# Performance work log

Hardware: AMD Instinct MI355X
Metric: run time of the kernel (lower is better)

Reference implementation:

```python
import jax, jax.numpy as jnp
import numpy as np

B, DIN, DOUT, NC = 8192, 4096, 4096, 64


def setup_inputs() -> dict:
    key = jax.random.key(0)
    k1, k2, k3, k4, k5 = jax.random.split(key, 5)
    x = jax.random.normal(k1, (B, DIN), dtype=jnp.float32)
    cluster = jax.random.uniform(k2, (B, NC), dtype=jnp.float32)
    weight = jax.random.uniform(k3, (DIN, DOUT), dtype=jnp.float32,
                                minval=-0.25, maxval=0.25)
    # torch init is ones; perturb slightly so the modulation is non-trivial
    style_L = 1.0 + 0.1 * jax.random.normal(k4, (NC, DIN), dtype=jnp.float32)
    style_R = 1.0 + 0.1 * jax.random.normal(k5, (NC, DOUT), dtype=jnp.float32)
    return {"x": x, "cluster": cluster, "weight": weight,
            "style_L": style_L, "style_R": style_R}


def reference(x, cluster, weight, style_L, style_R):
    # tmp_L: (B, din), tmp_R: (B, dout)
    tmp_L = cluster @ style_L
    tmp_R = cluster @ style_R
    # Algebraically identical to (weight * outer(tmp_L, tmp_R)) applied per
    # sample: out[b,o] = sum_i x[b,i]*tmpL[b,i]*W[i,o]*tmpR[b,o].
    # Factorized form avoids the (B, din, dout) intermediate.
    return ((x * tmp_L) @ weight) * tmp_R
```

## Files before the change

kernel.cpp:

```cpp
#include <hip/hip_runtime.h>
#include <cstdint>

#define BB   8192
#define DIN  4096
#define DOUT 4096
#define NCL  64

typedef __bf16 bf16;
typedef __attribute__((ext_vector_type(8)))  __bf16 bf16x8;
typedef __attribute__((ext_vector_type(4)))  float  f32x4;
typedef __attribute__((ext_vector_type(16))) float  f32x16;

#define GAS(p) (reinterpret_cast<uint32_t __attribute__((address_space(1)))*>(reinterpret_cast<uintptr_t>(p)))
#define LAS(p) (reinterpret_cast<uint32_t __attribute__((address_space(3)))*>(reinterpret_cast<uintptr_t>(p)))

#define WAITV(n)  asm volatile("s_waitcnt vmcnt(" #n ")" ::: "memory")
#define WAITLN(n) asm volatile("s_waitcnt lgkmcnt(" #n ")" ::: "memory")
#define WAITL()   asm volatile("s_waitcnt lgkmcnt(0)" ::: "memory")
#define BARR()    __builtin_amdgcn_s_barrier()
#define SCHED0()  __builtin_amdgcn_sched_barrier(0)
#define MFMA16(a, b, c) __builtin_amdgcn_mfma_f32_16x16x32_bf16((a), (b), (c), 0, 0, 0)
#define MFMA32(a, b, c) __builtin_amdgcn_mfma_f32_32x32x16_bf16((a), (b), (c), 0, 0, 0)

__global__ __launch_bounds__(256) void prologue_kernel(
    const float* __restrict__ x, const float* __restrict__ cl,
    const float* __restrict__ sL, bf16* __restrict__ Ap,
    bf16* __restrict__ clb)
{
    __shared__ uint4 lds_u4[2048];
    char* lds = (char*)lds_u4;
    const int t    = threadIdx.x;
    const int lane = t & 63;
    const int w    = t >> 6;
    const int wm   = w >> 1, wn = w & 1;
    const int r0   = blockIdx.x * 128;
    const int c0   = blockIdx.y * 128;

    #pragma unroll
    for (int i = 0; i < 4; i++) {
        int tk  = t + i * 256;
        int row = tk >> 3, ch = tk & 7;
        const float* src = cl + (size_t)(r0 + row) * NCL + ch * 8;
        float4 v0 = *(const float4*)src;
        float4 v1 = *(const float4*)(src + 4);
        bf16x8 pk;
        pk[0]=(bf16)v0.x; pk[1]=(bf16)v0.y; pk[2]=(bf16)v0.z; pk[3]=(bf16)v0.w;
        pk[4]=(bf16)v1.x; pk[5]=(bf16)v1.y; pk[6]=(bf16)v1.z; pk[7]=(bf16)v1.w;
        *(bf16x8*)(lds + row * 128 + ((ch ^ (row & 7)) << 4)) = pk;
        if (blockIdx.y == 0)
            *(bf16x8*)(clb + (size_t)(r0 + row) * NCL + ch * 8) = pk;
    }
    #pragma unroll
    for (int i = 0; i < 4; i++) {
        int tk = t + i * 256;
        int n  = tk & 127, c = tk >> 7;
        bf16x8 pl;
        #pragma unroll
        for (int j = 0; j < 8; j++)
            pl[j] = (bf16)sL[(size_t)(c * 8 + j) * DIN + c0 + n];
        *(bf16x8*)(lds + 16384 + n * 128 + ((c ^ (n & 7)) << 4)) = pl;
    }
    __syncthreads();

    f32x4 accL[4][4] = {};
    #pragma unroll
    for (int s = 0; s < 2; s++) {
        bf16x8 a[4], bl[4];
        #pragma unroll
        for (int m = 0; m < 4; m++) {
            int row = wm * 64 + m * 16 + (lane & 15);
            int ch  = s * 4 + (lane >> 4);
            a[m] = *(bf16x8*)(lds + row * 128 + ((ch ^ (row & 7)) << 4));
        }
        #pragma unroll
        for (int n = 0; n < 4; n++) {
            int row = wn * 64 + n * 16 + (lane & 15);
            int ch  = s * 4 + (lane >> 4);
            bl[n] = *(bf16x8*)(lds + 16384 + row * 128 + ((ch ^ (row & 7)) << 4));
        }
        #pragma unroll
        for (int m = 0; m < 4; m++)
            #pragma unroll
            for (int n = 0; n < 4; n++)
                accL[m][n] = MFMA16(a[m], bl[n], accL[m][n]);
    }

    #pragma unroll
    for (int m = 0; m < 4; m++) {
        int rbase = r0 + wm * 64 + m * 16 + ((lane >> 4) << 2);
        #pragma unroll
        for (int n = 0; n < 4; n++) {
            int col = c0 + wn * 64 + n * 16 + (lane & 15);
            #pragma unroll
            for (int j = 0; j < 4; j++) {
                size_t idx = (size_t)(rbase + j) * DIN + col;
                Ap[idx] = (bf16)(x[idx] * accL[m][n][j]);
            }
        }
    }
}

__global__ __launch_bounds__(256) void transpose_kernel(
    const float* __restrict__ W, bf16* __restrict__ Wt)
{
    const int t  = threadIdx.x;
    const int n  = blockIdx.x * 256 + t;
    const int k0 = blockIdx.y * 32;
    bf16x8 v[4];
    #pragma unroll
    for (int q = 0; q < 4; q++)
        #pragma unroll
        for (int j = 0; j < 8; j++)
            v[q][j] = (bf16)W[(size_t)(k0 + q * 8 + j) * DOUT + n];
    bf16* dst = Wt + (size_t)n * DIN + k0;
    #pragma unroll
    for (int q = 0; q < 4; q++)
        *(bf16x8*)(dst + q * 8) = v[q];
}

__global__ __launch_bounds__(256) void srt_kernel(
    const float* __restrict__ sR, bf16* __restrict__ srt)
{
    const int o = blockIdx.x * 256 + threadIdx.x;
    bf16x8 v[8];
    #pragma unroll
    for (int q = 0; q < 8; q++)
        #pragma unroll
        for (int j = 0; j < 8; j++)
            v[q][j] = (bf16)sR[(size_t)(q * 8 + j) * DOUT + o];
    bf16* dst = srt + (size_t)o * 64;
    #pragma unroll
    for (int q = 0; q < 8; q++)
        *(bf16x8*)(dst + q * 8) = v[q];
}

template<int CUR>
__device__ __forceinline__ void tile_step(char* lds, int tid,
    const bf16* pA1, const bf16* pA2, const bf16* pA3, const bf16* pA4,
    const bf16* pB1, const bf16* pB2, const bf16* pB3, const bf16* pB4,
    int kA1, int kA2, int arow, int brow,
    int ks0, int ks1, int ks2, int ks3,
    bf16x8 (&a)[2][4], bf16x8 (&b0)[4], bf16x8 (&b1)[4], f32x16 (&acc)[4][2])
{
    constexpr int CB = CUR * 65536;
    constexpr int OB = (CUR ^ 1) * 65536;
    const int ks[4] = {ks0, ks1, ks2, ks3};

    #pragma unroll
    for (int f = 0; f < 2; ++f)
        #pragma unroll
        for (int kk = 0; kk < 4; ++kk)
            a[f][kk] = *(const bf16x8*)(lds + CB + f * 4096 + arow + ks[kk]);
    #pragma unroll
    for (int kk = 0; kk < 4; ++kk)
        b0[kk] = *(const bf16x8*)(lds + CB + 32768 + brow + ks[kk]);
    __builtin_amdgcn_global_load_lds(GAS(pA3 + kA1), LAS(lds + OB + 16384 + tid * 16), 16, 0, 0);
    __builtin_amdgcn_global_load_lds(GAS(pA4 + kA1), LAS(lds + OB + 24576 + tid * 16), 16, 0, 0);
    WAITLN(8);
    BARR();
    WAITL(); SCHED0();
    __builtin_amdgcn_s_setprio(1);
    #pragma unroll
    for (int kk = 0; kk < 4; ++kk)
        #pragma unroll
        for (int f = 0; f < 2; ++f)
            acc[f][0] = MFMA32(a[f][kk], b0[kk], acc[f][0]);
    __builtin_amdgcn_s_setprio(0);
    BARR();

    #pragma unroll
    for (int kk = 0; kk < 4; ++kk)
        b1[kk] = *(const bf16x8*)(lds + CB + 49152 + brow + ks[kk]);
    __builtin_amdgcn_global_load_lds(GAS(pA1 + kA2), LAS(lds + CB + tid * 16), 16, 0, 0);
    __builtin_amdgcn_global_load_lds(GAS(pA2 + kA2), LAS(lds + CB + 8192 + tid * 16), 16, 0, 0);
    BARR();
    WAITL(); SCHED0();
    __builtin_amdgcn_s_setprio(1);
    #pragma unroll
    for (int kk = 0; kk < 4; ++kk)
        #pragma unroll
        for (int f = 0; f < 2; ++f)
            acc[f][1] = MFMA32(a[f][kk], b1[kk], acc[f][1]);
    __builtin_amdgcn_s_setprio(0);
    BARR();

    #pragma unroll
    for (int f = 0; f < 2; ++f)
        #pragma unroll
        for (int kk = 0; kk < 4; ++kk)
            a[f][kk] = *(const bf16x8*)(lds + CB + 16384 + f * 4096 + arow + ks[kk]);
    __builtin_amdgcn_global_load_lds(GAS(pB1 + kA2), LAS(lds + CB + 32768 + tid * 16), 16, 0, 0);
    __builtin_amdgcn_global_load_lds(GAS(pB2 + kA2), LAS(lds + CB + 40960 + tid * 16), 16, 0, 0);
    BARR();
    WAITL(); SCHED0();
    __builtin_amdgcn_s_setprio(1);
    #pragma unroll
    for (int kk = 0; kk < 4; ++kk)
        #pragma unroll
        for (int f = 0; f < 2; ++f)
            acc[2 + f][1] = MFMA32(a[f][kk], b1[kk], acc[2 + f][1]);
    __builtin_amdgcn_s_setprio(0);
    BARR();

    __builtin_amdgcn_global_load_lds(GAS(pB3 + kA2), LAS(lds + CB + 49152 + tid * 16), 16, 0, 0);
    __builtin_amdgcn_global_load_lds(GAS(pB4 + kA2), LAS(lds + CB + 57344 + tid * 16), 16, 0, 0);
    BARR();
    __builtin_amdgcn_s_setprio(1);
    #pragma unroll
    for (int kk = 0; kk < 4; ++kk)
        #pragma unroll
        for (int f = 0; f < 2; ++f)
            acc[2 + f][0] = MFMA32(a[f][kk], b0[kk], acc[2 + f][0]);
    __builtin_amdgcn_s_setprio(0);
    WAITV(6);
    BARR();
}

__global__ __launch_bounds__(512, 2) void gemm_kernel(
    const bf16* __restrict__ Ap, const bf16* __restrict__ Wt,
    const bf16* __restrict__ clb, const bf16* __restrict__ srt,
    float* __restrict__ out)
{
    __shared__ uint4 smem[8192];
    char* lds = (char*)smem;
    const int tid  = threadIdx.x;
    const int lane = tid & 63;
    const int w    = tid >> 6;
    const int wm   = w >> 2;
    const int wn   = w & 3;
    const int L5 = lane & 31, H1 = lane >> 5;

    const int bid = blockIdx.x;
    const int xc  = bid & 7, ii = bid >> 3;
    const int mt  = xc * 4 + (ii >> 4);
    const int nt  = ii & 15;
    const size_t brow_g = (size_t)mt * 256;
    const size_t bcol_g = (size_t)nt * 256;

    const int r1  = tid >> 3;
    const int gch = (tid & 7) ^ (r1 & 7);
    const bf16* pA1 = Ap + (brow_g + r1) * (size_t)DIN + gch * 8;
    const bf16* pA2 = pA1 + (size_t)64  * DIN;
    const bf16* pA3 = pA1 + (size_t)128 * DIN;
    const bf16* pA4 = pA1 + (size_t)192 * DIN;
    const bf16* pB1 = Wt + (bcol_g + r1) * (size_t)DIN + gch * 8;
    const bf16* pB2 = pB1 + (size_t)64  * DIN;
    const bf16* pB3 = pB1 + (size_t)128 * DIN;
    const bf16* pB4 = pB1 + (size_t)192 * DIN;

    const int ks0 = (((0 * 2 + H1) ^ (L5 & 7)) << 4);
    const int ks1 = (((1 * 2 + H1) ^ (L5 & 7)) << 4);
    const int ks2 = (((2 * 2 + H1) ^ (L5 & 7)) << 4);
    const int ks3 = (((3 * 2 + H1) ^ (L5 & 7)) << 4);
    const int arow = (wm * 64 + L5) * 128;
    const int brow = (wn * 32 + L5) * 128;

    bf16x8 a[2][4], b0[4], b1[4];
    f32x16 acc[4][2] = {};

    __builtin_amdgcn_global_load_lds(GAS(pA1), LAS(lds + tid * 16), 16, 0, 0);
    __builtin_amdgcn_global_load_lds(GAS(pA2), LAS(lds + 8192 + tid * 16), 16, 0, 0);
    __builtin_amdgcn_global_load_lds(GAS(pA3), LAS(lds + 16384 + tid * 16), 16, 0, 0);
    __builtin_amdgcn_global_load_lds(GAS(pA4), LAS(lds + 24576 + tid * 16), 16, 0, 0);
    __builtin_amdgcn_global_load_lds(GAS(pB1), LAS(lds + 32768 + tid * 16), 16, 0, 0);
    __builtin_amdgcn_global_load_lds(GAS(pB2), LAS(lds + 40960 + tid * 16), 16, 0, 0);
    __builtin_amdgcn_global_load_lds(GAS(pB3), LAS(lds + 49152 + tid * 16), 16, 0, 0);
    __builtin_amdgcn_global_load_lds(GAS(pB4), LAS(lds + 57344 + tid * 16), 16, 0, 0);
    __builtin_amdgcn_global_load_lds(GAS(pA1 + 64), LAS(lds + 65536 + tid * 16), 16, 0, 0);
    __builtin_amdgcn_global_load_lds(GAS(pA2 + 64), LAS(lds + 65536 + 8192 + tid * 16), 16, 0, 0);
    __builtin_amdgcn_global_load_lds(GAS(pB1 + 64), LAS(lds + 65536 + 32768 + tid * 16), 16, 0, 0);
    __builtin_amdgcn_global_load_lds(GAS(pB2 + 64), LAS(lds + 65536 + 40960 + tid * 16), 16, 0, 0);
    __builtin_amdgcn_global_load_lds(GAS(pB3 + 64), LAS(lds + 65536 + 49152 + tid * 16), 16, 0, 0);
    __builtin_amdgcn_global_load_lds(GAS(pB4 + 64), LAS(lds + 65536 + 57344 + tid * 16), 16, 0, 0);
    WAITV(6);
    BARR();

    #pragma unroll 1
    for (int t = 0; t < 64; t += 2) {
        tile_step<0>(lds, tid, pA1, pA2, pA3, pA4, pB1, pB2, pB3, pB4,
                     ((t + 1) & 63) * 64, ((t + 2) & 63) * 64,
                     arow, brow, ks0, ks1, ks2, ks3, a, b0, b1, acc);
        tile_step<1>(lds, tid, pA1, pA2, pA3, pA4, pB1, pB2, pB3, pB4,
                     ((t + 2) & 63) * 64, ((t + 3) & 63) * 64,
                     arow, brow, ks0, ks1, ks2, ks3, a, b0, b1, acc);
    }

    WAITV(0);
    const bf16* pC = clb + (brow_g + r1) * 64 + gch * 8;
    const bf16* pR = srt + (bcol_g + r1) * 64 + gch * 8;
    __builtin_amdgcn_global_load_lds(GAS(pC),         LAS(lds + tid * 16), 16, 0, 0);
    __builtin_amdgcn_global_load_lds(GAS(pC + 4096),  LAS(lds + 8192 + tid * 16), 16, 0, 0);
    __builtin_amdgcn_global_load_lds(GAS(pC + 8192),  LAS(lds + 16384 + tid * 16), 16, 0, 0);
    __builtin_amdgcn_global_load_lds(GAS(pC + 12288), LAS(lds + 24576 + tid * 16), 16, 0, 0);
    __builtin_amdgcn_global_load_lds(GAS(pR),         LAS(lds + 32768 + tid * 16), 16, 0, 0);
    __builtin_amdgcn_global_load_lds(GAS(pR + 4096),  LAS(lds + 40960 + tid * 16), 16, 0, 0);
    __builtin_amdgcn_global_load_lds(GAS(pR + 8192),  LAS(lds + 49152 + tid * 16), 16, 0, 0);
    __builtin_amdgcn_global_load_lds(GAS(pR + 12288), LAS(lds + 57344 + tid * 16), 16, 0, 0);
    WAITV(0);
    BARR();

    const int ks[4] = {ks0, ks1, ks2, ks3};
    bf16x8 cb[2][4];
    #pragma unroll
    for (int nf = 0; nf < 2; ++nf)
        #pragma unroll
        for (int kk = 0; kk < 4; ++kk)
            cb[nf][kk] = *(const bf16x8*)(lds + 32768 + (nf * 2 + (wn >> 1)) * 8192
                                          + ((wn & 1) * 32 + L5) * 128 + ks[kk]);
    #pragma unroll
    for (int mf = 0; mf < 4; ++mf) {
        bf16x8 ca[4];
        #pragma unroll
        for (int kk = 0; kk < 4; ++kk)
            ca[kk] = *(const bf16x8*)(lds + ((mf >> 1) * 2 + wm) * 8192
                                      + ((mf & 1) * 32 + L5) * 128 + ks[kk]);
        WAITL(); SCHED0();
        #pragma unroll
        for (int nf = 0; nf < 2; ++nf) {
            f32x16 r = {};
            #pragma unroll
            for (int kk = 0; kk < 4; ++kk)
                r = MFMA32(ca[kk], cb[nf][kk], r);
            acc[mf][nf] *= r;
        }
    }

    #pragma unroll
    for (int mf = 0; mf < 4; ++mf) {
        size_t rbase = brow_g + (size_t)((mf >> 1) * 128 + wm * 64 + (mf & 1) * 32 + 4 * H1);
        #pragma unroll
        for (int nf = 0; nf < 2; ++nf) {
            size_t col = bcol_g + (size_t)(nf * 128 + wn * 32 + L5);
            #pragma unroll
            for (int reg = 0; reg < 16; ++reg) {
                size_t row = rbase + (reg & 3) + 8 * (reg >> 2);
                out[row * DOUT + col] = acc[mf][nf][reg];
            }
        }
    }
}

extern "C" void kernel_launch(void* const* d_in, const int* in_sizes, int n_in,
                              void* d_out, int out_size, void* d_ws, size_t ws_size,
                              hipStream_t stream)
{
    (void)in_sizes; (void)n_in; (void)out_size;
    const float* x  = (const float*)d_in[0];
    const float* cl = (const float*)d_in[1];
    const float* W  = (const float*)d_in[2];
    const float* sL = (const float*)d_in[3];
    const float* sR = (const float*)d_in[4];
    float* out = (float*)d_out;

    const size_t AP_BYTES = (size_t)BB * DIN * sizeof(bf16);
    const size_t WT_BYTES = (size_t)DIN * DOUT * sizeof(bf16);
    const size_t CL_BYTES = (size_t)BB * NCL * sizeof(bf16);
    const size_t SR_BYTES = (size_t)DOUT * NCL * sizeof(bf16);
    if (ws_size < AP_BYTES + WT_BYTES + CL_BYTES + SR_BYTES) return;

    char* ws = (char*)d_ws;
    bf16* Ap  = (bf16*)ws;
    bf16* Wt  = (bf16*)(ws + AP_BYTES);
    bf16* clb = (bf16*)(ws + AP_BYTES + WT_BYTES);
    bf16* srt = (bf16*)(ws + AP_BYTES + WT_BYTES + CL_BYTES);

    prologue_kernel<<<dim3(BB / 128, DIN / 128), 256, 0, stream>>>(x, cl, sL, Ap, clb);
    transpose_kernel<<<dim3(DOUT / 256, DIN / 32), 256, 0, stream>>>(W, Wt);
    srt_kernel<<<dim3(DOUT / 256), 256, 0, stream>>>(sR, srt);
    gemm_kernel<<<dim3((BB / 256) * (DOUT / 256)), 512, 0, stream>>>(Ap, Wt, clb, srt, out);
}
```

Before: 365.4 us.

## Restructure GEMM LDS layout, barriers, tile mapping, and fuse prep kernels

The prologue now stages the modulation factors through LDS so the x*tmpL product is read and written as vectorised 8-wide rows instead of scalar strided accesses. The W transpose and style_R transpose kernels are merged into one launch. In the GEMM, LDS uses a k-major layout without XOR swizzle. Several intra-step barriers are dropped and the phase order is reshuffled. Block-to-tile mapping becomes 8x8 groups for L2 locality. These target prologue memory inefficiency, launch overhead and GEMM synchronisation stalls, but risk LDS bank conflicts from the removed swizzle and races from the removed barriers.

```diff
diff --git a/kernel.cpp b/kernel.cpp
--- a/kernel.cpp
+++ b/kernel.cpp
@@ -15,7 +15,6 @@
 #define LAS(p) (reinterpret_cast<uint32_t __attribute__((address_space(3)))*>(reinterpret_cast<uintptr_t>(p)))
 
 #define WAITV(n)  asm volatile("s_waitcnt vmcnt(" #n ")" ::: "memory")
-#define WAITLN(n) asm volatile("s_waitcnt lgkmcnt(" #n ")" ::: "memory")
 #define WAITL()   asm volatile("s_waitcnt lgkmcnt(0)" ::: "memory")
 #define BARR()    __builtin_amdgcn_s_barrier()
 #define SCHED0()  __builtin_amdgcn_sched_barrier(0)
@@ -27,8 +26,7 @@
     const float* __restrict__ sL, bf16* __restrict__ Ap,
     bf16* __restrict__ clb)
 {
-    __shared__ uint4 lds_u4[2048];
-    char* lds = (char*)lds_u4;
+    __shared__ char lds[34816];
     const int t    = threadIdx.x;
     const int lane = t & 63;
     const int w    = t >> 6;
@@ -84,61 +82,77 @@
             for (int n = 0; n < 4; n++)
                 accL[m][n] = MFMA16(a[m], bl[n], accL[m][n]);
     }
+    __syncthreads();
 
     #pragma unroll
     for (int m = 0; m < 4; m++) {
-        int rbase = r0 + wm * 64 + m * 16 + ((lane >> 4) << 2);
+        int rbase = wm * 64 + m * 16 + ((lane >> 4) << 2);
         #pragma unroll
         for (int n = 0; n < 4; n++) {
-            int col = c0 + wn * 64 + n * 16 + (lane & 15);
-            #pragma unroll
-            for (int j = 0; j < 4; j++) {
-                size_t idx = (size_t)(rbase + j) * DIN + col;
-                Ap[idx] = (bf16)(x[idx] * accL[m][n][j]);
-            }
-        }
-    }
-}
-
-__global__ __launch_bounds__(256) void transpose_kernel(
-    const float* __restrict__ W, bf16* __restrict__ Wt)
-{
-    const int t  = threadIdx.x;
-    const int n  = blockIdx.x * 256 + t;
-    const int k0 = blockIdx.y * 32;
-    bf16x8 v[4];
-    #pragma unroll
-    for (int q = 0; q < 4; q++)
-        #pragma unroll
-        for (int j = 0; j < 8; j++)
-            v[q][j] = (bf16)W[(size_t)(k0 + q * 8 + j) * DOUT + n];
-    bf16* dst = Wt + (size_t)n * DIN + k0;
-    #pragma unroll
-    for (int q = 0; q < 4; q++)
-        *(bf16x8*)(dst + q * 8) = v[q];
-}
-
-__global__ __launch_bounds__(256) void srt_kernel(
-    const float* __restrict__ sR, bf16* __restrict__ srt)
-{
-    const int o = blockIdx.x * 256 + threadIdx.x;
-    bf16x8 v[8];
-    #pragma unroll
-    for (int q = 0; q < 8; q++)
-        #pragma unroll
-        for (int j = 0; j < 8; j++)
-            v[q][j] = (bf16)sR[(size_t)(q * 8 + j) * DOUT + o];
-    bf16* dst = srt + (size_t)o * 64;
-    #pragma unroll
-    for (int q = 0; q < 8; q++)
-        *(bf16x8*)(dst + q * 8) = v[q];
+            int col = wn * 64 + n * 16 + (lane & 15);
+            #pragma unroll
+            for (int j = 0; j < 4; j++)
+                *(bf16*)(lds + (rbase + j) * 272 + col * 2) = (bf16)accL[m][n][j];
+        }
+    }
+    __syncthreads();
+
+    const int L = t & 15, H = (t >> 4) & 3;
+    #pragma unroll
+    for (int it = 0; it < 8; it++) {
+        int row = it * 16 + w * 4 + H;
+        bf16x8 tl = *(const bf16x8*)(lds + row * 272 + L * 16);
+        const float* xs = x + (size_t)(r0 + row) * DIN + c0 + L * 8;
+        float4 x0 = *(const float4*)xs;
+        float4 x1 = *(const float4*)(xs + 4);
+        bf16x8 o;
+        o[0]=(bf16)(x0.x*(float)tl[0]); o[1]=(bf16)(x0.y*(float)tl[1]);
+        o[2]=(bf16)(x0.z*(float)tl[2]); o[3]=(bf16)(x0.w*(float)tl[3]);
+        o[4]=(bf16)(x1.x*(float)tl[4]); o[5]=(bf16)(x1.y*(float)tl[5]);
+        o[6]=(bf16)(x1.z*(float)tl[6]); o[7]=(bf16)(x1.w*(float)tl[7]);
+        *(bf16x8*)(Ap + (size_t)(r0 + row) * DIN + c0 + L * 8) = o;
+    }
+}
+
+__global__ __launch_bounds__(256) void wprep_kernel(
+    const float* __restrict__ W, const float* __restrict__ sR,
+    bf16* __restrict__ Wt, bf16* __restrict__ srt)
+{
+    const int bid = blockIdx.x;
+    const int t   = threadIdx.x;
+    if (bid < 2048) {
+        const int n  = (bid & 15) * 256 + t;
+        const int k0 = (bid >> 4) * 32;
+        bf16x8 v[4];
+        #pragma unroll
+        for (int q = 0; q < 4; q++)
+            #pragma unroll
+            for (int j = 0; j < 8; j++)
+                v[q][j] = (bf16)W[(size_t)(k0 + q * 8 + j) * DOUT + n];
+        bf16* dst = Wt + (size_t)n * DIN + k0;
+        #pragma unroll
+        for (int q = 0; q < 4; q++)
+            *(bf16x8*)(dst + q * 8) = v[q];
+    } else {
+        const int o = (bid - 2048) * 256 + t;
+        bf16x8 v[8];
+        #pragma unroll
+        for (int q = 0; q < 8; q++)
+            #pragma unroll
+            for (int j = 0; j < 8; j++)
+                v[q][j] = (bf16)sR[(size_t)(q * 8 + j) * DOUT + o];
+        bf16* dst = srt + (size_t)o * 64;
+        #pragma unroll
+        for (int q = 0; q < 8; q++)
+            *(bf16x8*)(dst + q * 8) = v[q];
+    }
 }
 
 template<int CUR>
 __device__ __forceinline__ void tile_step(char* lds, int tid,
     const bf16* pA1, const bf16* pA2, const bf16* pA3, const bf16* pA4,
     const bf16* pB1, const bf16* pB2, const bf16* pB3, const bf16* pB4,
-    int kA1, int kA2, int arow, int brow,
+    int kA1, int kA2, int abase, int bbase,
     int ks0, int ks1, int ks2, int ks3,
     bf16x8 (&a)[2][4], bf16x8 (&b0)[4], bf16x8 (&b1)[4], f32x16 (&acc)[4][2])
 {
@@ -147,73 +161,72 @@
     const int ks[4] = {ks0, ks1, ks2, ks3};
 
     #pragma unroll
-    for (int f = 0; f < 2; ++f)
+    for (int mf = 0; mf < 2; ++mf)
         #pragma unroll
         for (int kk = 0; kk < 4; ++kk)
-            a[f][kk] = *(const bf16x8*)(lds + CB + f * 4096 + arow + ks[kk]);
-    #pragma unroll
-    for (int kk = 0; kk < 4; ++kk)
-        b0[kk] = *(const bf16x8*)(lds + CB + 32768 + brow + ks[kk]);
+            a[mf][kk] = *(const bf16x8*)(lds + CB + abase + mf * 512 + ks[kk]);
+    #pragma unroll
+    for (int kk = 0; kk < 4; ++kk)
+        b0[kk] = *(const bf16x8*)(lds + CB + bbase + ks[kk]);
     __builtin_amdgcn_global_load_lds(GAS(pA3 + kA1), LAS(lds + OB + 16384 + tid * 16), 16, 0, 0);
     __builtin_amdgcn_global_load_lds(GAS(pA4 + kA1), LAS(lds + OB + 24576 + tid * 16), 16, 0, 0);
-    WAITLN(8);
     BARR();
     WAITL(); SCHED0();
     __builtin_amdgcn_s_setprio(1);
     #pragma unroll
     for (int kk = 0; kk < 4; ++kk)
         #pragma unroll
-        for (int f = 0; f < 2; ++f)
-            acc[f][0] = MFMA32(a[f][kk], b0[kk], acc[f][0]);
+        for (int mf = 0; mf < 2; ++mf)
+            acc[mf][0] = MFMA32(a[mf][kk], b0[kk], acc[mf][0]);
     __builtin_amdgcn_s_setprio(0);
-    BARR();
-
-    #pragma unroll
-    for (int kk = 0; kk < 4; ++kk)
-        b1[kk] = *(const bf16x8*)(lds + CB + 49152 + brow + ks[kk]);
+    SCHED0();
+
+    #pragma unroll
+    for (int kk = 0; kk < 4; ++kk)
+        b1[kk] = *(const bf16x8*)(lds + CB + 16384 + bbase + ks[kk]);
+    __builtin_amdgcn_global_load_lds(GAS(pB1 + kA2), LAS(lds + CB + 32768 + tid * 16), 16, 0, 0);
+    __builtin_amdgcn_global_load_lds(GAS(pB2 + kA2), LAS(lds + CB + 40960 + tid * 16), 16, 0, 0);
+    BARR();
+    WAITL(); SCHED0();
+    __builtin_amdgcn_s_setprio(1);
+    #pragma unroll
+    for (int kk = 0; kk < 4; ++kk)
+        #pragma unroll
+        for (int mf = 0; mf < 2; ++mf)
+            acc[mf][1] = MFMA32(a[mf][kk], b1[kk], acc[mf][1]);
+    __builtin_amdgcn_s_setprio(0);
+    SCHED0();
+
+    #pragma unroll
+    for (int mf = 0; mf < 2; ++mf)
+        #pragma unroll
+        for (int kk = 0; kk < 4; ++kk)
+            a[mf][kk] = *(const bf16x8*)(lds + CB + 16384 + abase + mf * 512 + ks[kk]);
+    __builtin_amdgcn_global_load_lds(GAS(pB3 + kA2), LAS(lds + CB + 49152 + tid * 16), 16, 0, 0);
+    __builtin_amdgcn_global_load_lds(GAS(pB4 + kA2), LAS(lds + CB + 57344 + tid * 16), 16, 0, 0);
+    BARR();
+    WAITL(); SCHED0();
+    __builtin_amdgcn_s_setprio(1);
+    #pragma unroll
+    for (int kk = 0; kk < 4; ++kk)
+        #pragma unroll
+        for (int mf = 0; mf < 2; ++mf)
+            acc[2 + mf][1] = MFMA32(a[mf][kk], b1[kk], acc[2 + mf][1]);
+    __builtin_amdgcn_s_setprio(0);
+    SCHED0();
+
     __builtin_amdgcn_global_load_lds(GAS(pA1 + kA2), LAS(lds + CB + tid * 16), 16, 0, 0);
     __builtin_amdgcn_global_load_lds(GAS(pA2 + kA2), LAS(lds + CB + 8192 + tid * 16), 16, 0, 0);
-    BARR();
-    WAITL(); SCHED0();
+    WAITV(6);
+    BARR();
     __builtin_amdgcn_s_setprio(1);
     #pragma unroll
     for (int kk = 0; kk < 4; ++kk)
         #pragma unroll
-        for (int f = 0; f < 2; ++f)
-            acc[f][1] = MFMA32(a[f][kk], b1[kk], acc[f][1]);
+        for (int mf = 0; mf < 2; ++mf)
+            acc[2 + mf][0] = MFMA32(a[mf][kk], b0[kk], acc[2 + mf][0]);
     __builtin_amdgcn_s_setprio(0);
-    BARR();
-
-    #pragma unroll
-    for (int f = 0; f < 2; ++f)
-        #pragma unroll
-        for (int kk = 0; kk < 4; ++kk)
-            a[f][kk] = *(const bf16x8*)(lds + CB + 16384 + f * 4096 + arow + ks[kk]);
-    __builtin_amdgcn_global_load_lds(GAS(pB1 + kA2), LAS(lds + CB + 32768 + tid * 16), 16, 0, 0);
-    __builtin_amdgcn_global_load_lds(GAS(pB2 + kA2), LAS(lds + CB + 40960 + tid * 16), 16, 0, 0);
-    BARR();
-    WAITL(); SCHED0();
-    __builtin_amdgcn_s_setprio(1);
-    #pragma unroll
-    for (int kk = 0; kk < 4; ++kk)
-        #pragma unroll
-        for (int f = 0; f < 2; ++f)
-            acc[2 + f][1] = MFMA32(a[f][kk], b1[kk], acc[2 + f][1]);
-    __builtin_amdgcn_s_setprio(0);
-    BARR();
-
-    __builtin_amdgcn_global_load_lds(GAS(pB3 + kA2), LAS(lds + CB + 49152 + tid * 16), 16, 0, 0);
-    __builtin_amdgcn_global_load_lds(GAS(pB4 + kA2), LAS(lds + CB + 57344 + tid * 16), 16, 0, 0);
-    BARR();
-    __builtin_amdgcn_s_setprio(1);
-    #pragma unroll
-    for (int kk = 0; kk < 4; ++kk)
-        #pragma unroll
-        for (int f = 0; f < 2; ++f)
-            acc[2 + f][0] = MFMA32(a[f][kk], b0[kk], acc[2 + f][0]);
-    __builtin_amdgcn_s_setprio(0);
-    WAITV(6);
-    BARR();
+    SCHED0();
 }
 
 __global__ __launch_bounds__(512, 2) void gemm_kernel(
@@ -232,28 +245,28 @@
 
     const int bid = blockIdx.x;
     const int xc  = bid & 7, ii = bid >> 3;
-    const int mt  = xc * 4 + (ii >> 4);
-    const int nt  = ii & 15;
-    const size_t brow_g = (size_t)mt * 256;
-    const size_t bcol_g = (size_t)nt * 256;
-
-    const int r1  = tid >> 3;
-    const int gch = (tid & 7) ^ (r1 & 7);
-    const bf16* pA1 = Ap + (brow_g + r1) * (size_t)DIN + gch * 8;
+    const int mt  = (xc >> 1) * 8 + (ii >> 3);
+    const int nt  = (xc & 1) * 8 + (ii & 7);
+    const size_t brow = (size_t)mt * 256;
+    const size_t bcol = (size_t)nt * 256;
+
+    const int r6 = tid & 63;
+    const int ch = tid >> 6;
+    const bf16* pA1 = Ap + (brow + r6) * (size_t)DIN + ch * 8;
     const bf16* pA2 = pA1 + (size_t)64  * DIN;
     const bf16* pA3 = pA1 + (size_t)128 * DIN;
     const bf16* pA4 = pA1 + (size_t)192 * DIN;
-    const bf16* pB1 = Wt + (bcol_g + r1) * (size_t)DIN + gch * 8;
+    const bf16* pB1 = Wt + (bcol + r6) * (size_t)DIN + ch * 8;
     const bf16* pB2 = pB1 + (size_t)64  * DIN;
     const bf16* pB3 = pB1 + (size_t)128 * DIN;
     const bf16* pB4 = pB1 + (size_t)192 * DIN;
 
-    const int ks0 = (((0 * 2 + H1) ^ (L5 & 7)) << 4);
-    const int ks1 = (((1 * 2 + H1) ^ (L5 & 7)) << 4);
-    const int ks2 = (((2 * 2 + H1) ^ (L5 & 7)) << 4);
-    const int ks3 = (((3 * 2 + H1) ^ (L5 & 7)) << 4);
-    const int arow = (wm * 64 + L5) * 128;
-    const int brow = (wn * 32 + L5) * 128;
+    const int ks0 = ((0 * 2 + H1) << 10);
+    const int ks1 = ((1 * 2 + H1) << 10);
+    const int ks2 = ((2 * 2 + H1) << 10);
+    const int ks3 = ((3 * 2 + H1) << 10);
+    const int abase = wm * 8192 + L5 * 16;
+    const int bbase = 32768 + (wn >> 1) * 8192 + (wn & 1) * 512 + L5 * 16;
 
     bf16x8 a[2][4], b0[4], b1[4];
     f32x16 acc[4][2] = {};
@@ -266,12 +279,12 @@
     __builtin_amdgcn_global_load_lds(GAS(pB2), LAS(lds + 40960 + tid * 16), 16, 0, 0);
     __builtin_amdgcn_global_load_lds(GAS(pB3), LAS(lds + 49152 + tid * 16), 16, 0, 0);
     __builtin_amdgcn_global_load_lds(GAS(pB4), LAS(lds + 57344 + tid * 16), 16, 0, 0);
-    __builtin_amdgcn_global_load_lds(GAS(pA1 + 64), LAS(lds + 65536 + tid * 16), 16, 0, 0);
-    __builtin_amdgcn_global_load_lds(GAS(pA2 + 64), LAS(lds + 65536 + 8192 + tid * 16), 16, 0, 0);
     __builtin_amdgcn_global_load_lds(GAS(pB1 + 64), LAS(lds + 65536 + 32768 + tid * 16), 16, 0, 0);
     __builtin_amdgcn_global_load_lds(GAS(pB2 + 64), LAS(lds + 65536 + 40960 + tid * 16), 16, 0, 0);
     __builtin_amdgcn_global_load_lds(GAS(pB3 + 64), LAS(lds + 65536 + 49152 + tid * 16), 16, 0, 0);
     __builtin_amdgcn_global_load_lds(GAS(pB4 + 64), LAS(lds + 65536 + 57344 + tid * 16), 16, 0, 0);
+    __builtin_amdgcn_global_load_lds(GAS(pA1 + 64), LAS(lds + 65536 + tid * 16), 16, 0, 0);
+    __builtin_amdgcn_global_load_lds(GAS(pA2 + 64), LAS(lds + 65536 + 8192 + tid * 16), 16, 0, 0);
     WAITV(6);
     BARR();
 
@@ -279,23 +292,24 @@
     for (int t = 0; t < 64; t += 2) {
         tile_step<0>(lds, tid, pA1, pA2, pA3, pA4, pB1, pB2, pB3, pB4,
                      ((t + 1) & 63) * 64, ((t + 2) & 63) * 64,
-                     arow, brow, ks0, ks1, ks2, ks3, a, b0, b1, acc);
+                     abase, bbase, ks0, ks1, ks2, ks3, a, b0, b1, acc);
         tile_step<1>(lds, tid, pA1, pA2, pA3, pA4, pB1, pB2, pB3, pB4,
                      ((t + 2) & 63) * 64, ((t + 3) & 63) * 64,
-                     arow, brow, ks0, ks1, ks2, ks3, a, b0, b1, acc);
-    }
-
+                     abase, bbase, ks0, ks1, ks2, ks3, a, b0, b1, acc);
+    }
+
+    BARR();
     WAITV(0);
-    const bf16* pC = clb + (brow_g + r1) * 64 + gch * 8;
-    const bf16* pR = srt + (bcol_g + r1) * 64 + gch * 8;
-    __builtin_amdgcn_global_load_lds(GAS(pC),         LAS(lds + tid * 16), 16, 0, 0);
-    __builtin_amdgcn_global_load_lds(GAS(pC + 4096),  LAS(lds + 8192 + tid * 16), 16, 0, 0);
-    __builtin_amdgcn_global_load_lds(GAS(pC + 8192),  LAS(lds + 16384 + tid * 16), 16, 0, 0);
-    __builtin_amdgcn_global_load_lds(GAS(pC + 12288), LAS(lds + 24576 + tid * 16), 16, 0, 0);
-    __builtin_amdgcn_global_load_lds(GAS(pR),         LAS(lds + 32768 + tid * 16), 16, 0, 0);
-    __builtin_amdgcn_global_load_lds(GAS(pR + 4096),  LAS(lds + 40960 + tid * 16), 16, 0, 0);
-    __builtin_amdgcn_global_load_lds(GAS(pR + 8192),  LAS(lds + 49152 + tid * 16), 16, 0, 0);
-    __builtin_amdgcn_global_load_lds(GAS(pR + 12288), LAS(lds + 57344 + tid * 16), 16, 0, 0);
+    const bf16* pC = clb + (brow + r6) * 64 + ch * 8;
+    const bf16* pR = srt + (bcol + r6) * 64 + ch * 8;
+    __builtin_amdgcn_global_load_lds(GAS(pC),            LAS(lds + tid * 16), 16, 0, 0);
+    __builtin_amdgcn_global_load_lds(GAS(pC + 64 * 64),  LAS(lds + 8192 + tid * 16), 16, 0, 0);
+    __builtin_amdgcn_global_load_lds(GAS(pC + 128 * 64), LAS(lds + 16384 + tid * 16), 16, 0, 0);
+    __builtin_amdgcn_global_load_lds(GAS(pC + 192 * 64), LAS(lds + 24576 + tid * 16), 16, 0, 0);
+    __builtin_amdgcn_global_load_lds(GAS(pR),            LAS(lds + 32768 + tid * 16), 16, 0, 0);
+    __builtin_amdgcn_global_load_lds(GAS(pR + 64 * 64),  LAS(lds + 40960 + tid * 16), 16, 0, 0);
+    __builtin_amdgcn_global_load_lds(GAS(pR + 128 * 64), LAS(lds + 49152 + tid * 16), 16, 0, 0);
+    __builtin_amdgcn_global_load_lds(GAS(pR + 192 * 64), LAS(lds + 57344 + tid * 16), 16, 0, 0);
     WAITV(0);
     BARR();
 
@@ -306,14 +320,14 @@
         #pragma unroll
         for (int kk = 0; kk < 4; ++kk)
             cb[nf][kk] = *(const bf16x8*)(lds + 32768 + (nf * 2 + (wn >> 1)) * 8192
-                                          + ((wn & 1) * 32 + L5) * 128 + ks[kk]);
+                                          + (wn & 1) * 512 + L5 * 16 + ks[kk]);
     #pragma unroll
     for (int mf = 0; mf < 4; ++mf) {
         bf16x8 ca[4];
         #pragma unroll
         for (int kk = 0; kk < 4; ++kk)
             ca[kk] = *(const bf16x8*)(lds + ((mf >> 1) * 2 + wm) * 8192
-                                      + ((mf & 1) * 32 + L5) * 128 + ks[kk]);
+                                      + (mf & 1) * 512 + L5 * 16 + ks[kk]);
         WAITL(); SCHED0();
         #pragma unroll
         for (int nf = 0; nf < 2; ++nf) {
@@ -327,10 +341,10 @@
 
     #pragma unroll
     for (int mf = 0; mf < 4; ++mf) {
-        size_t rbase = brow_g + (size_t)((mf >> 1) * 128 + wm * 64 + (mf & 1) * 32 + 4 * H1);
+        size_t rbase = brow + (size_t)((mf >> 1) * 128 + wm * 64 + (mf & 1) * 32 + 4 * H1);
         #pragma unroll
         for (int nf = 0; nf < 2; ++nf) {
-            size_t col = bcol_g + (size_t)(nf * 128 + wn * 32 + L5);
+            size_t col = bcol + (size_t)(nf * 128 + wn * 32 + L5);
             #pragma unroll
             for (int reg = 0; reg < 16; ++reg) {
                 size_t row = rbase + (reg & 3) + 8 * (reg >> 2);
@@ -365,7 +379,6 @@
     bf16* srt = (bf16*)(ws + AP_BYTES + WT_BYTES + CL_BYTES);
 
     prologue_kernel<<<dim3(BB / 128, DIN / 128), 256, 0, stream>>>(x, cl, sL, Ap, clb);
-    transpose_kernel<<<dim3(DOUT / 256, DIN / 32), 256, 0, stream>>>(W, Wt);
-    srt_kernel<<<dim3(DOUT / 256), 256, 0, stream>>>(sR, srt);
+    wprep_kernel<<<dim3(2064), 256, 0, stream>>>(W, sR, Wt, srt);
     gemm_kernel<<<dim3((BB / 256) * (DOUT / 256)), 512, 0, stream>>>(Ap, Wt, clb, srt, out);
 }
```

Measured after the change: 374.7 us. +2.5%, slower.
